# Optimization experiments

Hardware: AMD Instinct MI355X
Metric: run time of the kernel (lower is better)

Reference implementation:

```python
import jax, jax.numpy as jnp
import numpy as np

B, S, D, H = 2, 2048, 1024, 16
HD = D // H  # 64


def setup_inputs() -> dict:
    key = jax.random.key(0)
    ks = jax.random.split(key, 10)
    s = 1.0 / np.sqrt(D)
    X = jax.random.normal(ks[0], (B, S, D), dtype=jnp.float32)
    # pad the last 256 key positions (nonzero = ignore); causal rows still
    # attend to earlier unpadded keys so no all-masked rows.
    kpm = jnp.broadcast_to((jnp.arange(S) >= S - 256).astype(jnp.int32), (B, S))
    return {
        "X": X,
        "key_padding_mask": kpm,
        "Wq": jax.random.uniform(ks[1], (D, D), jnp.float32, -s, s),
        "bq": jax.random.uniform(ks[2], (D,), jnp.float32, -s, s),
        "Wk": jax.random.uniform(ks[3], (D, D), jnp.float32, -s, s),
        "bk": jax.random.uniform(ks[4], (D,), jnp.float32, -s, s),
        "Wv": jax.random.uniform(ks[5], (D, D), jnp.float32, -s, s),
        "bv": jax.random.uniform(ks[6], (D,), jnp.float32, -s, s),
        "Wo": jax.random.uniform(ks[7], (D, D), jnp.float32, -s, s),
        "bo": jax.random.uniform(ks[8], (D,), jnp.float32, -s, s),
    }


def _mha(X, kpm, Wq, bq, Wk, bk, Wv, bv, Wo, bo):
    b, s, d = X.shape
    def heads(t):  # (b,s,d) -> (b,H,s,hd)
        return t.reshape(b, s, H, HD).transpose(0, 2, 1, 3)
    Q = heads(X @ Wq.T + bq)
    K = heads(X @ Wk.T + bk)
    V = heads(X @ Wv.T + bv)
    scores = jnp.einsum('bhqd,bhkd->bhqk', Q, K) / jnp.sqrt(jnp.float32(HD))
    causal = jnp.triu(jnp.ones((s, s), dtype=bool), k=1)  # True above diag
    scores = jnp.where(causal[None, None], -jnp.inf, scores)
    scores = jnp.where(kpm[:, None, None, :] != 0, -jnp.inf, scores)
    A = jax.nn.softmax(scores, axis=-1)
    out = jnp.einsum('bhqk,bhkd->bhqd', A, V)  # (b,H,s,hd)
    out = out.transpose(0, 2, 1, 3).reshape(b, s, d)
    return out @ Wo.T + bo


def reference(X, key_padding_mask, Wq, bq, Wk, bk, Wv, bv, Wo, bo):
    return _mha(X, key_padding_mask, Wq, bq, Wk, bk, Wv, bv, Wo, bo)
```

## Files before the change

kernel.cpp:

```cpp
#include <hip/hip_runtime.h>
#include <math.h>

#define DEV __device__ __forceinline__

typedef __attribute__((ext_vector_type(4))) float f32x4;
typedef __attribute__((ext_vector_type(8))) __bf16 bf16x8;

static constexpr int Bc = 2, Sc = 2048, Dc = 1024, Hc = 16, HDc = 64;
static constexpr int LDQ = 3 * Dc;
static constexpr float SCL = 0.125f * 1.44269504f;

DEV unsigned short f2b(float f) {
  union { float f; unsigned int u; } c; c.f = f;
  unsigned int u = c.u;
  unsigned int r = (u + 0x7fffu + ((u >> 16) & 1u)) >> 16;
  return (unsigned short)r;
}

DEV void async16(const void* g, void* l) {
  __builtin_amdgcn_global_load_lds(
      (__attribute__((address_space(1))) void*)(void*)g,
      (__attribute__((address_space(3))) void*)l, 16, 0, 0);
}

DEV int swz(int r, int c) { return r * 64 + (c ^ ((r & 7) << 3)); }

__global__ void cvt_x(const float* __restrict__ in,
                      unsigned short* __restrict__ out, int n4) {
  int i = blockIdx.x * blockDim.x + threadIdx.x;
  if (i < n4) {
    const float4 v = reinterpret_cast<const float4*>(in)[i];
    ushort4 o;
    o.x = f2b(v.x); o.y = f2b(v.y); o.z = f2b(v.z); o.w = f2b(v.w);
    reinterpret_cast<ushort4*>(out)[i] = o;
  }
}

__global__ void cvt_w(const float* __restrict__ w0, const float* __restrict__ w1,
                      const float* __restrict__ w2, const float* __restrict__ w3,
                      unsigned short* __restrict__ out) {
  const float* src = blockIdx.y == 0 ? w0
                     : blockIdx.y == 1 ? w1
                     : blockIdx.y == 2 ? w2 : w3;
  const int i = blockIdx.x * blockDim.x + threadIdx.x;
  const float4 v = reinterpret_cast<const float4*>(src)[i];
  ushort4 o;
  o.x = f2b(v.x); o.y = f2b(v.y); o.z = f2b(v.z); o.w = f2b(v.w);
  reinterpret_cast<ushort4*>(out)[(size_t)blockIdx.y * (Dc * Dc / 4) + i] = o;
}

template <typename OUT>
__global__ __launch_bounds__(256, 2) void gemm_bt(
    const unsigned short* __restrict__ A, const unsigned short* __restrict__ Bm,
    const float* __restrict__ b0, const float* __restrict__ b1,
    const float* __restrict__ b2, OUT* __restrict__ C, int M, int K, int ldc) {
  __shared__ unsigned short As[128 * 64];
  __shared__ unsigned short Bs[128 * 64];
  const int tid = threadIdx.x;
  const int wave = tid >> 6, lane = tid & 63;
  const int wr = wave >> 1, wc = wave & 1;
  const int row0 = blockIdx.x * 128, col0 = blockIdx.y * 128;
  const int srow = lane >> 3, scol = (lane & 7) * 8;

  f32x4 acc[4][4];
#pragma unroll
  for (int m = 0; m < 4; ++m)
#pragma unroll
    for (int n = 0; n < 4; ++n) acc[m][n] = {0.f, 0.f, 0.f, 0.f};

  for (int k0 = 0; k0 < K; k0 += 64) {
    __syncthreads();
#pragma unroll
    for (int c = 0; c < 4; ++c) {
      const int rr = (wave * 4 + c) * 8 + srow;
      async16(A + (size_t)(row0 + rr) * K + k0 + scol,
              (char*)As + (wave * 4 + c) * 1024);
      async16(Bm + (size_t)(col0 + rr) * K + k0 + scol,
              (char*)Bs + (wave * 4 + c) * 1024);
    }
    __syncthreads();
#pragma unroll
    for (int ks = 0; ks < 2; ++ks) {
      const int kk = ks * 32 + (lane >> 4) * 8;
      bf16x8 af[4], bfr[4];
#pragma unroll
      for (int m = 0; m < 4; ++m)
        af[m] = *reinterpret_cast<const bf16x8*>(
            &As[(wr * 64 + m * 16 + (lane & 15)) * 64 + kk]);
#pragma unroll
      for (int n = 0; n < 4; ++n)
        bfr[n] = *reinterpret_cast<const bf16x8*>(
            &Bs[(wc * 64 + n * 16 + (lane & 15)) * 64 + kk]);
#pragma unroll
      for (int m = 0; m < 4; ++m)
#pragma unroll
        for (int n = 0; n < 4; ++n)
          acc[m][n] = __builtin_amdgcn_mfma_f32_16x16x32_bf16(af[m], bfr[n],
                                                              acc[m][n], 0, 0, 0);
    }
  }
  const int r4 = (lane >> 4) * 4, cl = lane & 15;
#pragma unroll
  for (int n = 0; n < 4; ++n) {
    const int gc = col0 + wc * 64 + n * 16 + cl;
    const float* bp = gc < Dc ? b0 : (gc < 2 * Dc ? b1 : b2);
    const float bv = bp[gc & (Dc - 1)];
#pragma unroll
    for (int m = 0; m < 4; ++m) {
#pragma unroll
      for (int j = 0; j < 4; ++j) {
        const int gr = row0 + wr * 64 + m * 16 + r4 + j;
        const float v = acc[m][n][j] + bv;
        if constexpr (sizeof(OUT) == 4)
          C[(size_t)gr * ldc + gc] = v;
        else
          C[(size_t)gr * ldc + gc] = (OUT)f2b(v);
      }
    }
  }
}

__global__ __launch_bounds__(256, 4) void attn_fwd(
    const __bf16* __restrict__ Qg, const __bf16* __restrict__ Kg,
    const __bf16* __restrict__ Vg, const int* __restrict__ kpm,
    __bf16* __restrict__ Og) {
  __shared__ __bf16 QP[64 * 64];
  __shared__ __bf16 Ks[2][64 * 64];
  __shared__ __bf16 Vt[2][64 * 64];

  const int L = blockIdx.x;
  const int s = L >> 8, c = L & 255;
  const int u = c >> 5, bh = c & 31;
  const int qb = s * 8 + ((s & 1) ? (7 - u) : u);

  const int b = bh >> 4, h = bh & 15;
  const int q0 = qb * 64;
  const int tid = threadIdx.x, wave = tid >> 6, lane = tid & 63;
  const size_t base = (size_t)b * Sc * LDQ + (size_t)h * HDc;
  const int srow = lane >> 3;
  const int scol = 8 * ((lane & 7) ^ srow);
  const int hi = lane >> 4, cl = lane & 15, r4 = hi * 4;

  const int vk2 = (tid & 31) * 2, vd8 = (tid >> 5) * 8;
  const __bf16* vbase = Vg + base + (size_t)vk2 * LDQ + vd8;
  const int* mbase = kpm + b * Sc;

  union VV { uint4 q; unsigned short u[8]; };

#pragma unroll
  for (int cc = 0; cc < 2; ++cc) {
    const int rr = (wave * 2 + cc) * 8 + srow;
    async16(Qg + base + (size_t)(q0 + rr) * LDQ + scol,
            (char*)QP + (wave * 2 + cc) * 1024);
    async16(Kg + base + (size_t)rr * LDQ + scol,
            (char*)Ks[0] + (wave * 2 + cc) * 1024);
  }
  VV v0, v1;
  v0.q = *reinterpret_cast<const uint4*>(vbase);
  v1.q = *reinterpret_cast<const uint4*>(vbase + LDQ);
  int mki[4];
#pragma unroll
  for (int n = 0; n < 4; ++n) mki[n] = mbase[n * 16 + cl];
  {
    unsigned int* V32 = reinterpret_cast<unsigned int*>(Vt[0]);
#pragma unroll
    for (int i = 0; i < 8; ++i) {
      const int row = vd8 + i;
      V32[row * 32 + ((tid & 31) ^ ((row & 7) << 2))] =
          (unsigned int)v0.u[i] | ((unsigned int)v1.u[i] << 16);
    }
  }
  __syncthreads();

  bf16x8 qf[2];
#pragma unroll
  for (int ks = 0; ks < 2; ++ks)
    qf[ks] = *reinterpret_cast<const bf16x8*>(
        &QP[swz(wave * 16 + cl, ks * 32 + hi * 8)]);
  __bf16* Ps = QP + wave * 1024;

  bf16x8 ones;
#pragma unroll
  for (int i = 0; i < 8; ++i) ones[i] = (__bf16)1.0f;

  f32x4 o[4], lacc;
  float m_[4];
#pragma unroll
  for (int n = 0; n < 4; ++n) o[n] = {0.f, 0.f, 0.f, 0.f};
  lacc = {0.f, 0.f, 0.f, 0.f};
#pragma unroll
  for (int j = 0; j < 4; ++j) m_[j] = -1e30f;

  int pb = 0;
  for (int kb = 0; kb <= qb; ++kb) {
    const bool diag = (kb == qb);
    VV n0, n1;
    int nmk[4];
    if (!diag) {
      const int k1 = (kb + 1) * 64;
#pragma unroll
      for (int cc = 0; cc < 2; ++cc) {
        const int rr = (wave * 2 + cc) * 8 + srow;
        async16(Kg + base + (size_t)(k1 + rr) * LDQ + scol,
                (char*)Ks[pb ^ 1] + (wave * 2 + cc) * 1024);
      }
      n0.q = *reinterpret_cast<const uint4*>(vbase + (size_t)k1 * LDQ);
      n1.q = *reinterpret_cast<const uint4*>(vbase + (size_t)(k1 + 1) * LDQ);
#pragma unroll
      for (int n = 0; n < 4; ++n) nmk[n] = mbase[k1 + n * 16 + cl];
    }

    f32x4 sa[4];
#pragma unroll
    for (int n = 0; n < 4; ++n) sa[n] = {0.f, 0.f, 0.f, 0.f};
    __builtin_amdgcn_s_setprio(1);
#pragma unroll
    for (int ks = 0; ks < 2; ++ks) {
      const int kk = ks * 32 + hi * 8;
#pragma unroll
      for (int n = 0; n < 4; ++n) {
        if (!(diag && n > wave)) {
          const bf16x8 kf = *reinterpret_cast<const bf16x8*>(
              &Ks[pb][swz(n * 16 + cl, kk)]);
          sa[n] = __builtin_amdgcn_mfma_f32_16x16x32_bf16(qf[ks], kf, sa[n],
                                                          0, 0, 0);
        }
      }
    }
    __builtin_amdgcn_s_setprio(0);
    float pm[4] = {-1e30f, -1e30f, -1e30f, -1e30f};
#pragma unroll
    for (int n = 0; n < 4; ++n) {
      const float mf = mki[n] ? -1e30f : 0.0f;
#pragma unroll
      for (int j = 0; j < 4; ++j) {
        float s2 = fmaf(sa[n][j], SCL, mf);
        if (diag && (kb * 64 + n * 16 + cl > q0 + wave * 16 + r4 + j))
          s2 = -1e30f;
        sa[n][j] = s2;
        pm[j] = fmaxf(pm[j], s2);
      }
    }
    const bool ok = (pm[0] - m_[0] <= 8.f) && (pm[1] - m_[1] <= 8.f) &&
                    (pm[2] - m_[2] <= 8.f) && (pm[3] - m_[3] <= 8.f);
    if (!__all(ok)) {
#pragma unroll
      for (int off = 1; off < 16; off <<= 1)
#pragma unroll
        for (int j = 0; j < 4; ++j)
          pm[j] = fmaxf(pm[j], __shfl_xor(pm[j], off, 64));
#pragma unroll
      for (int j = 0; j < 4; ++j) {
        const float mn = fmaxf(m_[j], pm[j]);
        const float sc = __builtin_amdgcn_exp2f(m_[j] - mn);
        m_[j] = mn;
        lacc[j] *= sc;
#pragma unroll
        for (int n = 0; n < 4; ++n) o[n][j] *= sc;
      }
    }
#pragma unroll
    for (int n = 0; n < 4; ++n)
#pragma unroll
      for (int j = 0; j < 4; ++j) {
        const float p = __builtin_amdgcn_exp2f(sa[n][j] - m_[j]);
        Ps[swz(r4 + j, n * 16 + cl)] = (__bf16)p;
      }
    __builtin_amdgcn_s_setprio(1);
#pragma unroll
    for (int ks = 0; ks < 2; ++ks) {
      const int kk = ks * 32 + hi * 8;
      const bf16x8 pf = *reinterpret_cast<const bf16x8*>(&Ps[swz(cl, kk)]);
#pragma unroll
      for (int n = 0; n < 4; ++n) {
        const bf16x8 vf = *reinterpret_cast<const bf16x8*>(
            &Vt[pb][swz(n * 16 + cl, kk)]);
        o[n] = __builtin_amdgcn_mfma_f32_16x16x32_bf16(pf, vf, o[n], 0, 0, 0);
      }
      lacc = __builtin_amdgcn_mfma_f32_16x16x32_bf16(pf, ones, lacc, 0, 0, 0);
    }
    __builtin_amdgcn_s_setprio(0);
    if (!diag) {
      unsigned int* V32 = reinterpret_cast<unsigned int*>(Vt[pb ^ 1]);
#pragma unroll
      for (int i = 0; i < 8; ++i) {
        const int row = vd8 + i;
        V32[row * 32 + ((tid & 31) ^ ((row & 7) << 2))] =
            (unsigned int)n0.u[i] | ((unsigned int)n1.u[i] << 16);
      }
#pragma unroll
      for (int n = 0; n < 4; ++n) mki[n] = nmk[n];
    }
    __syncthreads();
    pb ^= 1;
  }

#pragma unroll
  for (int j = 0; j < 4; ++j) {
    const float inv = 1.f / lacc[j];
#pragma unroll
    for (int n = 0; n < 4; ++n)
      Og[(size_t)(b * Sc + q0 + wave * 16 + r4 + j) * Dc + h * HDc + n * 16 +
         cl] = (__bf16)(o[n][j] * inv);
  }
}

extern "C" void kernel_launch(void* const* d_in, const int* in_sizes, int n_in,
                              void* d_out, int out_size, void* d_ws,
                              size_t ws_size, hipStream_t stream) {
  const float* X = (const float*)d_in[0];
  const int* kpm = (const int*)d_in[1];
  const float* Wq = (const float*)d_in[2];
  const float* bq = (const float*)d_in[3];
  const float* Wk = (const float*)d_in[4];
  const float* bk = (const float*)d_in[5];
  const float* Wv = (const float*)d_in[6];
  const float* bv = (const float*)d_in[7];
  const float* Wo = (const float*)d_in[8];
  const float* bo = (const float*)d_in[9];
  float* out = (float*)d_out;

  char* w = (char*)d_ws;
  unsigned short* Xb = (unsigned short*)(w);
  unsigned short* Wqkvb = (unsigned short*)(w + (8u << 20));
  unsigned short* Wob = (unsigned short*)(w + (14u << 20));
  unsigned short* QKVb = (unsigned short*)(w + (16u << 20));
  unsigned short* Ab = (unsigned short*)(w + (40u << 20));

  const int MD = Bc * Sc;
  cvt_x<<<dim3(MD * Dc / 1024), 256, 0, stream>>>(X, Xb, MD * Dc / 4);
  cvt_w<<<dim3(Dc * Dc / 1024, 4), 256, 0, stream>>>(Wq, Wk, Wv, Wo, Wqkvb);

  gemm_bt<unsigned short><<<dim3(MD / 128, LDQ / 128), 256, 0, stream>>>(
      Xb, Wqkvb, bq, bk, bv, QKVb, MD, Dc, LDQ);

  attn_fwd<<<dim3(1024), 256, 0, stream>>>(
      (const __bf16*)QKVb, (const __bf16*)QKVb + Dc,
      (const __bf16*)QKVb + 2 * Dc, kpm, (__bf16*)Ab);

  gemm_bt<float><<<dim3(MD / 128, Dc / 128), 256, 0, stream>>>(
      Ab, Wob, bo, bo, bo, out, MD, Dc, Dc);
}
```

Baseline: 121.9 us.

## Process 128 query rows per attention block sharing each K/V tile

The attention kernel now uses 512-thread blocks covering two 64-row query tiles, so each K/V tile loaded into LDS is reused by eight waves instead of four. This halves K/V global traffic and the number of blocks. The waves of the lower query tile sit idle during the last key block, and the grid has fewer, larger blocks, which may lower occupancy and load balance.

```diff
diff --git a/kernel.cpp b/kernel.cpp
--- a/kernel.cpp
+++ b/kernel.cpp
@@ -120,52 +120,56 @@
   }
 }
 
-__global__ __launch_bounds__(256, 4) void attn_fwd(
+__global__ __launch_bounds__(512, 4) void attn_fwd(
     const __bf16* __restrict__ Qg, const __bf16* __restrict__ Kg,
     const __bf16* __restrict__ Vg, const int* __restrict__ kpm,
     __bf16* __restrict__ Og) {
-  __shared__ __bf16 QP[64 * 64];
+  __shared__ __bf16 QP[128 * 64];
   __shared__ __bf16 Ks[2][64 * 64];
   __shared__ __bf16 Vt[2][64 * 64];
 
   const int L = blockIdx.x;
   const int s = L >> 8, c = L & 255;
   const int u = c >> 5, bh = c & 31;
-  const int qb = s * 8 + ((s & 1) ? (7 - u) : u);
+  const int g = s * 8 + ((s & 1) ? (7 - u) : u);
 
   const int b = bh >> 4, h = bh & 15;
-  const int q0 = qb * 64;
+  const int q0 = g * 128;
   const int tid = threadIdx.x, wave = tid >> 6, lane = tid & 63;
+  const int wsub = wave & 3;
+  const int myqb = 2 * g + (wave >> 2);
+  const int kmax = 2 * g + 1;
   const size_t base = (size_t)b * Sc * LDQ + (size_t)h * HDc;
   const int srow = lane >> 3;
   const int scol = 8 * ((lane & 7) ^ srow);
   const int hi = lane >> 4, cl = lane & 15, r4 = hi * 4;
-
-  const int vk2 = (tid & 31) * 2, vd8 = (tid >> 5) * 8;
-  const __bf16* vbase = Vg + base + (size_t)vk2 * LDQ + vd8;
+  const int myq = q0 + (wave >> 2) * 64 + wsub * 16 + r4;
+
+  const int vk2 = (tid & 31) * 2, vd4 = (tid >> 5) * 4;
+  const __bf16* vbase = Vg + base + (size_t)vk2 * LDQ + vd4;
   const int* mbase = kpm + b * Sc;
 
-  union VV { uint4 q; unsigned short u[8]; };
+  union VV { uint2 q; unsigned short u[4]; };
 
 #pragma unroll
   for (int cc = 0; cc < 2; ++cc) {
     const int rr = (wave * 2 + cc) * 8 + srow;
     async16(Qg + base + (size_t)(q0 + rr) * LDQ + scol,
             (char*)QP + (wave * 2 + cc) * 1024);
-    async16(Kg + base + (size_t)rr * LDQ + scol,
-            (char*)Ks[0] + (wave * 2 + cc) * 1024);
-  }
+  }
+  async16(Kg + base + (size_t)(wave * 8 + srow) * LDQ + scol,
+          (char*)Ks[0] + wave * 1024);
   VV v0, v1;
-  v0.q = *reinterpret_cast<const uint4*>(vbase);
-  v1.q = *reinterpret_cast<const uint4*>(vbase + LDQ);
+  v0.q = *reinterpret_cast<const uint2*>(vbase);
+  v1.q = *reinterpret_cast<const uint2*>(vbase + LDQ);
   int mki[4];
 #pragma unroll
   for (int n = 0; n < 4; ++n) mki[n] = mbase[n * 16 + cl];
   {
     unsigned int* V32 = reinterpret_cast<unsigned int*>(Vt[0]);
 #pragma unroll
-    for (int i = 0; i < 8; ++i) {
-      const int row = vd8 + i;
+    for (int i = 0; i < 4; ++i) {
+      const int row = vd4 + i;
       V32[row * 32 + ((tid & 31) ^ ((row & 7) << 2))] =
           (unsigned int)v0.u[i] | ((unsigned int)v1.u[i] << 16);
     }
@@ -192,99 +196,98 @@
   for (int j = 0; j < 4; ++j) m_[j] = -1e30f;
 
   int pb = 0;
-  for (int kb = 0; kb <= qb; ++kb) {
-    const bool diag = (kb == qb);
+  for (int kb = 0; kb <= kmax; ++kb) {
+    const bool last = (kb == kmax);
     VV n0, n1;
     int nmk[4];
-    if (!diag) {
+    if (!last) {
       const int k1 = (kb + 1) * 64;
-#pragma unroll
-      for (int cc = 0; cc < 2; ++cc) {
-        const int rr = (wave * 2 + cc) * 8 + srow;
-        async16(Kg + base + (size_t)(k1 + rr) * LDQ + scol,
-                (char*)Ks[pb ^ 1] + (wave * 2 + cc) * 1024);
-      }
-      n0.q = *reinterpret_cast<const uint4*>(vbase + (size_t)k1 * LDQ);
-      n1.q = *reinterpret_cast<const uint4*>(vbase + (size_t)(k1 + 1) * LDQ);
+      async16(Kg + base + (size_t)(k1 + wave * 8 + srow) * LDQ + scol,
+              (char*)Ks[pb ^ 1] + wave * 1024);
+      n0.q = *reinterpret_cast<const uint2*>(vbase + (size_t)k1 * LDQ);
+      n1.q = *reinterpret_cast<const uint2*>(vbase + (size_t)(k1 + 1) * LDQ);
 #pragma unroll
       for (int n = 0; n < 4; ++n) nmk[n] = mbase[k1 + n * 16 + cl];
     }
 
-    f32x4 sa[4];
-#pragma unroll
-    for (int n = 0; n < 4; ++n) sa[n] = {0.f, 0.f, 0.f, 0.f};
-    __builtin_amdgcn_s_setprio(1);
-#pragma unroll
-    for (int ks = 0; ks < 2; ++ks) {
-      const int kk = ks * 32 + hi * 8;
+    if (kb <= myqb) {
+      const bool diag = (kb == myqb);
+      f32x4 sa[4];
+#pragma unroll
+      for (int n = 0; n < 4; ++n) sa[n] = {0.f, 0.f, 0.f, 0.f};
+      __builtin_amdgcn_s_setprio(1);
+#pragma unroll
+      for (int ks = 0; ks < 2; ++ks) {
+        const int kk = ks * 32 + hi * 8;
+#pragma unroll
+        for (int n = 0; n < 4; ++n) {
+          if (!(diag && n > wsub)) {
+            const bf16x8 kf = *reinterpret_cast<const bf16x8*>(
+                &Ks[pb][swz(n * 16 + cl, kk)]);
+            sa[n] = __builtin_amdgcn_mfma_f32_16x16x32_bf16(qf[ks], kf, sa[n],
+                                                            0, 0, 0);
+          }
+        }
+      }
+      __builtin_amdgcn_s_setprio(0);
+      float pm[4] = {-1e30f, -1e30f, -1e30f, -1e30f};
 #pragma unroll
       for (int n = 0; n < 4; ++n) {
-        if (!(diag && n > wave)) {
-          const bf16x8 kf = *reinterpret_cast<const bf16x8*>(
-              &Ks[pb][swz(n * 16 + cl, kk)]);
-          sa[n] = __builtin_amdgcn_mfma_f32_16x16x32_bf16(qf[ks], kf, sa[n],
-                                                          0, 0, 0);
-        }
-      }
-    }
-    __builtin_amdgcn_s_setprio(0);
-    float pm[4] = {-1e30f, -1e30f, -1e30f, -1e30f};
-#pragma unroll
-    for (int n = 0; n < 4; ++n) {
-      const float mf = mki[n] ? -1e30f : 0.0f;
-#pragma unroll
-      for (int j = 0; j < 4; ++j) {
-        float s2 = fmaf(sa[n][j], SCL, mf);
-        if (diag && (kb * 64 + n * 16 + cl > q0 + wave * 16 + r4 + j))
-          s2 = -1e30f;
-        sa[n][j] = s2;
-        pm[j] = fmaxf(pm[j], s2);
-      }
-    }
-    const bool ok = (pm[0] - m_[0] <= 8.f) && (pm[1] - m_[1] <= 8.f) &&
-                    (pm[2] - m_[2] <= 8.f) && (pm[3] - m_[3] <= 8.f);
-    if (!__all(ok)) {
-#pragma unroll
-      for (int off = 1; off < 16; off <<= 1)
-#pragma unroll
-        for (int j = 0; j < 4; ++j)
-          pm[j] = fmaxf(pm[j], __shfl_xor(pm[j], off, 64));
-#pragma unroll
-      for (int j = 0; j < 4; ++j) {
-        const float mn = fmaxf(m_[j], pm[j]);
-        const float sc = __builtin_amdgcn_exp2f(m_[j] - mn);
-        m_[j] = mn;
-        lacc[j] *= sc;
-#pragma unroll
-        for (int n = 0; n < 4; ++n) o[n][j] *= sc;
-      }
-    }
-#pragma unroll
-    for (int n = 0; n < 4; ++n)
-#pragma unroll
-      for (int j = 0; j < 4; ++j) {
-        const float p = __builtin_amdgcn_exp2f(sa[n][j] - m_[j]);
-        Ps[swz(r4 + j, n * 16 + cl)] = (__bf16)p;
-      }
-    __builtin_amdgcn_s_setprio(1);
-#pragma unroll
-    for (int ks = 0; ks < 2; ++ks) {
-      const int kk = ks * 32 + hi * 8;
-      const bf16x8 pf = *reinterpret_cast<const bf16x8*>(&Ps[swz(cl, kk)]);
-#pragma unroll
-      for (int n = 0; n < 4; ++n) {
-        const bf16x8 vf = *reinterpret_cast<const bf16x8*>(
-            &Vt[pb][swz(n * 16 + cl, kk)]);
-        o[n] = __builtin_amdgcn_mfma_f32_16x16x32_bf16(pf, vf, o[n], 0, 0, 0);
-      }
-      lacc = __builtin_amdgcn_mfma_f32_16x16x32_bf16(pf, ones, lacc, 0, 0, 0);
-    }
-    __builtin_amdgcn_s_setprio(0);
-    if (!diag) {
+        const float mf = mki[n] ? -1e30f : 0.0f;
+#pragma unroll
+        for (int j = 0; j < 4; ++j) {
+          float s2 = fmaf(sa[n][j], SCL, mf);
+          if (diag && (kb * 64 + n * 16 + cl > myq + j)) s2 = -1e30f;
+          sa[n][j] = s2;
+          pm[j] = fmaxf(pm[j], s2);
+        }
+      }
+      const bool ok = (pm[0] - m_[0] <= 8.f) && (pm[1] - m_[1] <= 8.f) &&
+                      (pm[2] - m_[2] <= 8.f) && (pm[3] - m_[3] <= 8.f);
+      if (!__all(ok)) {
+#pragma unroll
+        for (int off = 1; off < 16; off <<= 1)
+#pragma unroll
+          for (int j = 0; j < 4; ++j)
+            pm[j] = fmaxf(pm[j], __shfl_xor(pm[j], off, 64));
+#pragma unroll
+        for (int j = 0; j < 4; ++j) {
+          const float mn = fmaxf(m_[j], pm[j]);
+          const float sc = __builtin_amdgcn_exp2f(m_[j] - mn);
+          m_[j] = mn;
+          lacc[j] *= sc;
+#pragma unroll
+          for (int n = 0; n < 4; ++n) o[n][j] *= sc;
+        }
+      }
+#pragma unroll
+      for (int n = 0; n < 4; ++n)
+#pragma unroll
+        for (int j = 0; j < 4; ++j) {
+          const float p = __builtin_amdgcn_exp2f(sa[n][j] - m_[j]);
+          Ps[swz(r4 + j, n * 16 + cl)] = (__bf16)p;
+        }
+      __builtin_amdgcn_s_setprio(1);
+#pragma unroll
+      for (int ks = 0; ks < 2; ++ks) {
+        const int kk = ks * 32 + hi * 8;
+        const bf16x8 pf = *reinterpret_cast<const bf16x8*>(&Ps[swz(cl, kk)]);
+#pragma unroll
+        for (int n = 0; n < 4; ++n) {
+          const bf16x8 vf = *reinterpret_cast<const bf16x8*>(
+              &Vt[pb][swz(n * 16 + cl, kk)]);
+          o[n] = __builtin_amdgcn_mfma_f32_16x16x32_bf16(pf, vf, o[n], 0, 0, 0);
+        }
+        lacc = __builtin_amdgcn_mfma_f32_16x16x32_bf16(pf, ones, lacc, 0, 0, 0);
+      }
+      __builtin_amdgcn_s_setprio(0);
+    }
+
+    if (!last) {
       unsigned int* V32 = reinterpret_cast<unsigned int*>(Vt[pb ^ 1]);
 #pragma unroll
-      for (int i = 0; i < 8; ++i) {
-        const int row = vd8 + i;
+      for (int i = 0; i < 4; ++i) {
+        const int row = vd4 + i;
         V32[row * 32 + ((tid & 31) ^ ((row & 7) << 2))] =
             (unsigned int)n0.u[i] | ((unsigned int)n1.u[i] << 16);
       }
@@ -300,8 +303,8 @@
     const float inv = 1.f / lacc[j];
 #pragma unroll
     for (int n = 0; n < 4; ++n)
-      Og[(size_t)(b * Sc + q0 + wave * 16 + r4 + j) * Dc + h * HDc + n * 16 +
-         cl] = (__bf16)(o[n][j] * inv);
+      Og[(size_t)(b * Sc + myq + j) * Dc + h * HDc + n * 16 + cl] =
+          (__bf16)(o[n][j] * inv);
   }
 }
 
@@ -334,7 +337,7 @@
   gemm_bt<unsigned short><<<dim3(MD / 128, LDQ / 128), 256, 0, stream>>>(
       Xb, Wqkvb, bq, bk, bv, QKVb, MD, Dc, LDQ);
 
-  attn_fwd<<<dim3(1024), 256, 0, stream>>>(
+  attn_fwd<<<dim3(512), 512, 0, stream>>>(
       (const __bf16*)QKVb, (const __bf16*)QKVb + Dc,
       (const __bf16*)QKVb + 2 * Dc, kpm, (__bf16*)Ab);
 
```

Result: slower. 145.7 us (+19.5%).
